# Kernel optimization log

Hardware: AMD Instinct MI355X
Metric: run time of the kernel (lower is better)

## Reference

```python
import jax, jax.numpy as jnp
import numpy as np

B, NN, NC, CARD = 2048, 24, 8, 16
D, H, L, FH, K, DOUT = 512, 8, 3, 1024, 64, 1
S = NN + NC + 1  # M features + CLS token (appended last)
DH = D // H


def _ln(x, w, b):
    m = x.mean(-1, keepdims=True)
    v = ((x - m) ** 2).mean(-1, keepdims=True)
    return (x - m) / jnp.sqrt(v + 1e-5) * w + b


def _build_masks():
    # k random feature-feature interaction pairs per block (seed = attention_seed + block),
    # plus the diagonal and full CLS row/column (CLS is the last token).
    masks = np.zeros((L, S, S), dtype=bool)
    for l in range(L):
        rng = np.random.default_rng(42 + l)
        m = np.zeros((S, S), dtype=bool)
        np.fill_diagonal(m, True)
        m[S - 1, :] = True
        m[:, S - 1] = True
        M = S - 1
        for _ in range(K):
            i, j = rng.integers(0, M, size=2)
            m[i, j] = True
            m[j, i] = True
        masks[l] = m
    return jnp.asarray(masks)


def setup_inputs() -> dict:
    key = jax.random.key(0)
    cnt = [0]

    def nrm(shape, scale=0.02):
        cnt[0] += 1
        return jax.random.normal(jax.random.fold_in(key, cnt[0]), shape, jnp.float32) * scale

    inp = {}
    inp["x_num"] = jax.random.normal(jax.random.fold_in(key, 1000), (B, NN), jnp.float32)
    inp["x_cat"] = jax.random.randint(jax.random.fold_in(key, 1001), (B, NC), 0, CARD)
    # FeatureTokenizer params
    inp["w_num"] = nrm((NN, D), 0.1)
    inp["b_num"] = nrm((NN, D), 0.1)
    inp["emb_cat"] = nrm((NC * CARD, D), 0.1)
    inp["b_cat"] = nrm((NC, D), 0.1)
    inp["cls"] = nrm((D,), 0.1)
    # block params stacked over L blocks
    inp["ln1_w"] = jnp.ones((L, D)); inp["ln1_b"] = jnp.zeros((L, D))
    inp["Wq"] = nrm((L, D, D)); inp["bq"] = jnp.zeros((L, D))
    inp["Wk"] = nrm((L, D, D)); inp["bk"] = jnp.zeros((L, D))
    inp["Wv"] = nrm((L, D, D)); inp["bv"] = jnp.zeros((L, D))
    inp["Wo"] = nrm((L, D, D)); inp["bo"] = jnp.zeros((L, D))
    inp["ln2_w"] = jnp.ones((L, D)); inp["ln2_b"] = jnp.zeros((L, D))
    inp["Wf1"] = nrm((L, D, 2 * FH)); inp["bf1"] = jnp.zeros((L, 2 * FH))
    inp["Wf2"] = nrm((L, FH, D)); inp["bf2"] = jnp.zeros((L, D))
    inp["mask"] = _build_masks()
    inp["cat_offsets"] = jnp.arange(NC) * CARD
    # head params
    inp["hln_w"] = jnp.ones((D,)); inp["hln_b"] = jnp.zeros((D,))
    inp["Wh"] = nrm((D, DOUT)); inp["bh"] = jnp.zeros((DOUT,))
    return inp


def reference(x_num, x_cat, w_num, b_num, emb_cat, b_cat, cls, ln1_w, ln1_b, Wq, bq, Wk, bk, Wv, bv, Wo, bo, ln2_w, ln2_b, Wf1, bf1, Wf2, bf2, mask, cat_offsets, hln_w, hln_b, Wh, bh):
    b = x_num.shape[0]
    tok_num = x_num[:, :, None] * w_num[None] + b_num[None]          # [B, NN, D]
    tok_cat = emb_cat[x_cat + cat_offsets[None]] + b_cat[None]       # [B, NC, D]
    x = jnp.concatenate([tok_num, tok_cat, jnp.broadcast_to(cls, (b, 1, D))], axis=1)  # [B, S, D]
    scale = 1.0 / jnp.sqrt(jnp.asarray(DH, x.dtype))
    for l in range(L):
        # sparse random attention (prenorm)
        h = _ln(x, ln1_w[l], ln1_b[l])
        q = (h @ Wq[l] + bq[l]).reshape(b, S, H, DH)
        k = (h @ Wk[l] + bk[l]).reshape(b, S, H, DH)
        v = (h @ Wv[l] + bv[l]).reshape(b, S, H, DH)
        scores = jnp.einsum('bihd,bjhd->bhij', q, k) * scale
        scores = jnp.where(mask[l][None, None], scores, jnp.asarray(-1e9, scores.dtype))
        attn = jax.nn.softmax(scores, axis=-1)
        o = jnp.einsum('bhij,bjhd->bihd', attn, v).reshape(b, S, D)
        x = x + (o @ Wo[l] + bo[l])
        # ReGLU FFN (prenorm)
        h = _ln(x, ln2_w[l], ln2_b[l])
        f = h @ Wf1[l] + bf1[l]
        a, g = jnp.split(f, 2, axis=-1)
        x = x + ((a * jax.nn.relu(g)) @ Wf2[l] + bf2[l])
    # head on CLS token (last position): LayerNorm -> ReLU -> Linear
    c = _ln(x[:, -1], hln_w, hln_b)
    return jax.nn.relu(c) @ Wh + bh
```

## Files before the change

### kernel.cpp

```cpp
#include <hip/hip_runtime.h>
#include <stdint.h>

#define Bq    2048
#define NNq   24
#define NCq   8
#define CARDq 16
#define Dq    512
#define Hq    8
#define Lq    3
#define FHq   1024
#define Sq    33

typedef unsigned short u16;
typedef unsigned int   u32;
typedef __bf16 bf16x8 __attribute__((ext_vector_type(8)));
typedef float  f32x4  __attribute__((ext_vector_type(4)));

__device__ __forceinline__ u16 f2bf(float f) {
  return __builtin_bit_cast(u16, (__bf16)f);
}
__device__ __forceinline__ float bf2f(u16 h) {
  u32 u = ((u32)h) << 16;
  return __builtin_bit_cast(float, u);
}

__device__ __forceinline__ void glds16(const void* g, void* l) {
  __builtin_amdgcn_global_load_lds((const __attribute__((address_space(1))) void*)g,
                                   (__attribute__((address_space(3))) void*)l, 16, 0, 0);
}

__global__ __launch_bounds__(256) void wconv_all_kernel(const float* __restrict__ Wq,
                                                        const float* __restrict__ Wk,
                                                        const float* __restrict__ Wv,
                                                        const float* __restrict__ Wo,
                                                        const float* __restrict__ Wf1,
                                                        const float* __restrict__ Wf2,
                                                        u16* __restrict__ WqkvT,
                                                        u16* __restrict__ WoT,
                                                        u16* __restrict__ Wf1T,
                                                        u16* __restrict__ Wf2T) {
  __shared__ float tile[32][33];
  const int l = blockIdx.y;
  int id = blockIdx.x;
  const float* src; u16* dst; int K, N;
  if (id < 768) {
    const int m = id >> 8; id &= 255;
    src = ((m == 0) ? Wq : (m == 1) ? Wk : Wv) + (size_t)l * 262144;
    dst = WqkvT + (size_t)l * 786432 + (size_t)m * 262144;
    K = 512; N = 512;
  } else if (id < 1024) {
    id -= 768;
    src = Wo + (size_t)l * 262144;  dst = WoT + (size_t)l * 262144;
    K = 512; N = 512;
  } else if (id < 2048) {
    id -= 1024;
    src = Wf1 + (size_t)l * 1048576; dst = Wf1T + (size_t)l * 1048576;
    K = 512; N = 2048;
  } else {
    id -= 2048;
    src = Wf2 + (size_t)l * 524288;  dst = Wf2T + (size_t)l * 524288;
    K = 1024; N = 512;
  }
  const int ntn = N >> 5;
  const int n0 = (id % ntn) * 32, k0 = (id / ntn) * 32;
  const int tx = threadIdx.x & 31, ty = threadIdx.x >> 5;
#pragma unroll
  for (int r = 0; r < 32; r += 8)
    tile[ty + r][tx] = src[(size_t)(k0 + ty + r) * N + (n0 + tx)];
  __syncthreads();
#pragma unroll
  for (int r = 0; r < 32; r += 8)
    dst[(size_t)(n0 + ty + r) * K + (k0 + tx)] = f2bf(tile[tx][ty + r]);
}

__global__ __launch_bounds__(256) void maskf_kernel(const void* __restrict__ maskp,
                                                    float* __restrict__ maskF) {
  __shared__ int u8flag;
  const int l = blockIdx.x;
  const unsigned char* mu = (const unsigned char*)maskp + (size_t)l * (Sq * Sq);
  const int* mi = (const int*)maskp + (size_t)l * (Sq * Sq);
  if (threadIdx.x == 0) {
    int ok = 1;
    for (int i = 0; i < Sq; i++) ok &= (mu[i * (Sq + 1)] != 0) ? 1 : 0;
    u8flag = ok;
  }
  __syncthreads();
  const int use_u8 = u8flag;
  float* out = maskF + (size_t)l * 2304;
  for (int t = threadIdx.x; t < 2304; t += 256) {
    const int i = t / 48, j = t - i * 48;
    float v = -1e9f;
    if (i < Sq && j < Sq) {
      const int mv = use_u8 ? (int)mu[i * Sq + j] : mi[i * Sq + j];
      v = mv ? 0.f : -1e9f;
    }
    out[t] = v;
  }
}

__global__ __launch_bounds__(256) void tok_ln_kernel(const float* __restrict__ x_num,
                                                     const int* __restrict__ x_cat,
                                                     const float* __restrict__ w_num,
                                                     const float* __restrict__ b_num,
                                                     const float* __restrict__ emb_cat,
                                                     const float* __restrict__ b_cat,
                                                     const float* __restrict__ cls,
                                                     const float* __restrict__ gw,
                                                     const float* __restrict__ gb,
                                                     float* __restrict__ X,
                                                     u16* __restrict__ Hout, int c0) {
  const int wave = threadIdx.x >> 6, lane = threadIdx.x & 63;
  const int tok = blockIdx.x * 4 + wave;
  const int b   = tok / Sq;
  const int s   = tok - b * Sq;
  const int bg  = c0 + b;
  const int col0 = lane * 8;
  float v[8];
  if (s < NNq) {
    const float xv = x_num[bg * NNq + s];
    const float4 w0 = *(const float4*)(w_num + s * Dq + col0);
    const float4 w1 = *(const float4*)(w_num + s * Dq + col0 + 4);
    const float4 b0 = *(const float4*)(b_num + s * Dq + col0);
    const float4 b1 = *(const float4*)(b_num + s * Dq + col0 + 4);
    v[0]=fmaf(xv,w0.x,b0.x); v[1]=fmaf(xv,w0.y,b0.y); v[2]=fmaf(xv,w0.z,b0.z); v[3]=fmaf(xv,w0.w,b0.w);
    v[4]=fmaf(xv,w1.x,b1.x); v[5]=fmaf(xv,w1.y,b1.y); v[6]=fmaf(xv,w1.z,b1.z); v[7]=fmaf(xv,w1.w,b1.w);
  } else if (s < NNq + NCq) {
    const int j = s - NNq;
    const int row = x_cat[bg * NCq + j] + j * CARDq;
    const float4 e0 = *(const float4*)(emb_cat + (size_t)row * Dq + col0);
    const float4 e1 = *(const float4*)(emb_cat + (size_t)row * Dq + col0 + 4);
    const float4 b0 = *(const float4*)(b_cat + j * Dq + col0);
    const float4 b1 = *(const float4*)(b_cat + j * Dq + col0 + 4);
    v[0]=e0.x+b0.x; v[1]=e0.y+b0.y; v[2]=e0.z+b0.z; v[3]=e0.w+b0.w;
    v[4]=e1.x+b1.x; v[5]=e1.y+b1.y; v[6]=e1.z+b1.z; v[7]=e1.w+b1.w;
  } else {
    const float4 c0v = *(const float4*)(cls + col0);
    const float4 c1v = *(const float4*)(cls + col0 + 4);
    v[0]=c0v.x; v[1]=c0v.y; v[2]=c0v.z; v[3]=c0v.w;
    v[4]=c1v.x; v[5]=c1v.y; v[6]=c1v.z; v[7]=c1v.w;
  }
  float s1 = 0.f, s2 = 0.f;
#pragma unroll
  for (int i = 0; i < 8; i++) { s1 += v[i]; s2 += v[i] * v[i]; }
#pragma unroll
  for (int off = 32; off > 0; off >>= 1) { s1 += __shfl_xor(s1, off); s2 += __shfl_xor(s2, off); }
  const float mean = s1 * (1.0f / Dq);
  const float rstd = rsqrtf(s2 * (1.0f / Dq) - mean * mean + 1e-5f);
  float* xp = X + (size_t)tok * Dq + col0;
  *(float4*)xp       = (float4){v[0], v[1], v[2], v[3]};
  *(float4*)(xp + 4) = (float4){v[4], v[5], v[6], v[7]};
  const float* gwp = gw + col0;
  const float* gbp = gb + col0;
  u16 o[8];
#pragma unroll
  for (int i = 0; i < 8; i++) o[i] = f2bf((v[i] - mean) * rstd * gwp[i] + gbp[i]);
  uint4 pk;
  pk.x = (u32)o[0] | ((u32)o[1] << 16); pk.y = (u32)o[2] | ((u32)o[3] << 16);
  pk.z = (u32)o[4] | ((u32)o[5] << 16); pk.w = (u32)o[6] | ((u32)o[7] << 16);
  *(uint4*)(Hout + (size_t)tok * Dq + col0) = pk;
}

__global__ __launch_bounds__(256) void ln_kernel(const float* __restrict__ X,
                                                 const float* __restrict__ gw,
                                                 const float* __restrict__ gb,
                                                 u16* __restrict__ Hout,
                                                 int inmul, int inadd) {
  const int wave = threadIdx.x >> 6, lane = threadIdx.x & 63;
  const int row = blockIdx.x * 4 + wave;
  const size_t srow = (size_t)row * inmul + inadd;
  const float* xr = X + srow * Dq + lane * 8;
  const float4 a = *(const float4*)xr;
  const float4 b = *(const float4*)(xr + 4);
  float s  = a.x + a.y + a.z + a.w + b.x + b.y + b.z + b.w;
  float ss = a.x*a.x + a.y*a.y + a.z*a.z + a.w*a.w + b.x*b.x + b.y*b.y + b.z*b.z + b.w*b.w;
#pragma unroll
  for (int off = 32; off > 0; off >>= 1) { s += __shfl_xor(s, off); ss += __shfl_xor(ss, off); }
  const float mean = s * (1.0f / Dq);
  const float rstd = rsqrtf(ss * (1.0f / Dq) - mean * mean + 1e-5f);
  const float xv[8] = {a.x, a.y, a.z, a.w, b.x, b.y, b.z, b.w};
  const float* gwp = gw + lane * 8;
  const float* gbp = gb + lane * 8;
  u16 o[8];
#pragma unroll
  for (int i = 0; i < 8; i++) o[i] = f2bf((xv[i] - mean) * rstd * gwp[i] + gbp[i]);
  uint4 pk;
  pk.x = (u32)o[0] | ((u32)o[1] << 16); pk.y = (u32)o[2] | ((u32)o[3] << 16);
  pk.z = (u32)o[4] | ((u32)o[5] << 16); pk.w = (u32)o[6] | ((u32)o[7] << 16);
  *(uint4*)(Hout + (size_t)row * Dq + lane * 8) = pk;
}

template <int MODE>
__global__ __launch_bounds__(256) void gemm_kernel(const u16* __restrict__ A,
                                                   const u16* __restrict__ Bt0, const u16* __restrict__ Bt1, const u16* __restrict__ Bt2,
                                                   const float* __restrict__ bi0, const float* __restrict__ bi1, const float* __restrict__ bi2,
                                                   void* __restrict__ out0, void* __restrict__ out1, void* __restrict__ out2,
                                                   size_t ostride, int K, int amul, int aadd, int xmul, int xadd, int nofs) {
  __shared__ uint4 smem4[1024];
  char* smem = (char*)smem4;
  const int tid  = threadIdx.x;
  const int wave = tid >> 6;
  const int lane = tid & 63;
  const int mblk = blockIdx.y;
  const int nblk = blockIdx.x;
  const u16*   Bt;
  const float* bias;
  void*        outp;
  if (MODE == 3) {
    Bt = Bt0; bias = nullptr; outp = out0;
  } else {
    const int z = blockIdx.z;
    Bt   = (z == 0) ? Bt0 : (z == 1) ? Bt1 : Bt2;
    bias = (z == 0) ? bi0 : (z == 1) ? bi1 : bi2;
    outp = (z == 0) ? out0 : (z == 1) ? out1 : out2;
  }

  const int cg   = (lane & 3) ^ ((lane >> 3) & 3);
  const int arow = wave * 32 + (lane >> 2);
  const u16* gA0 = A + ((size_t)(mblk * 128 + arow) * amul + aadd) * K + cg * 8;
  const u16* gA1 = A + ((size_t)(mblk * 128 + arow + 16) * amul + aadd) * K + cg * 8;
  char* lA0 = smem + wave * 2048;
  char* lA1 = lA0 + 1024;

  const u16 *gB0, *gB1;
  char *lB0, *lB1;
  if (MODE == 2) {
    const int brow = wave * 16 + (lane >> 2);
    gB0 = Bt + (size_t)(nblk * 64 + brow) * K + cg * 8;
    gB1 = Bt + (size_t)(FHq + nblk * 64 + brow) * K + cg * 8;
    lB0 = smem + 8192  + wave * 1024;
    lB1 = smem + 12288 + wave * 1024;
  } else {
    const int brow = wave * 32 + (lane >> 2);
    gB0 = Bt + (size_t)((nblk + nofs) * 128 + brow) * K + cg * 8;
    gB1 = gB0 + (size_t)16 * K;
    lB0 = smem + 8192 + wave * 2048;
    lB1 = lB0 + 1024;
  }

  const int slot = (lane >> 4) ^ ((lane >> 1) & 3);
  const int r16  = lane & 15;
  const int wm   = (wave >> 1) * 64;
  int aoff[4], boff[4];
#pragma unroll
  for (int i = 0; i < 4; i++) aoff[i] = (wm + i * 16 + r16) * 64 + slot * 16;
  if (MODE == 2) {
    const int wn = (wave & 1) * 32;
#pragma unroll
    for (int j = 0; j < 2; j++) {
      boff[j]     = 8192  + (wn + j * 16 + r16) * 64 + slot * 16;
      boff[2 + j] = 12288 + (wn + j * 16 + r16) * 64 + slot * 16;
    }
  } else {
    const int wn = (wave & 1) * 64;
#pragma unroll
    for (int j = 0; j < 4; j++) boff[j] = 8192 + (wn + j * 16 + r16) * 64 + slot * 16;
  }

  f32x4 acc[16];
#pragma unroll
  for (int i = 0; i < 16; i++) acc[i] = (f32x4){0.f, 0.f, 0.f, 0.f};

  const int kiter = K >> 5;
  for (int kk = 0; kk < kiter; kk++) {
    __syncthreads();
    glds16(gA0, lA0); glds16(gA1, lA1);
    glds16(gB0, lB0); glds16(gB1, lB1);
    gA0 += 32; gA1 += 32; gB0 += 32; gB1 += 32;
    __syncthreads();

    if (MODE == 2) {
      bf16x8 af[4], ba[2], bg[2];
#pragma unroll
      for (int i = 0; i < 4; i++) af[i] = *(const bf16x8*)(smem + aoff[i]);
#pragma unroll
      for (int j = 0; j < 2; j++) {
        ba[j] = *(const bf16x8*)(smem + boff[j]);
        bg[j] = *(const bf16x8*)(smem + boff[2 + j]);
      }
#pragma unroll
      for (int i = 0; i < 4; i++)
#pragma unroll
        for (int j = 0; j < 2; j++) {
          acc[i * 2 + j]     = __builtin_amdgcn_mfma_f32_16x16x32_bf16(af[i], ba[j], acc[i * 2 + j], 0, 0, 0);
          acc[8 + i * 2 + j] = __builtin_amdgcn_mfma_f32_16x16x32_bf16(af[i], bg[j], acc[8 + i * 2 + j], 0, 0, 0);
        }
    } else {
      bf16x8 af[4], bf[4];
#pragma unroll
      for (int i = 0; i < 4; i++) af[i] = *(const bf16x8*)(smem + aoff[i]);
#pragma unroll
      for (int j = 0; j < 4; j++) bf[j] = *(const bf16x8*)(smem + boff[j]);
#pragma unroll
      for (int i = 0; i < 4; i++)
#pragma unroll
        for (int j = 0; j < 4; j++)
          acc[i * 4 + j] = __builtin_amdgcn_mfma_f32_16x16x32_bf16(af[i], bf[j], acc[i * 4 + j], 0, 0, 0);
    }
  }

  const int quad = lane >> 4;
  if (MODE == 3) {
    const int nb   = nblk + nofs;
    const int buf  = nb >> 2;
    u16* C = (u16*)out0 + (size_t)buf * ostride;
    const float* biasp = (buf == 0) ? bi0 : (buf == 1) ? bi1 : bi2;
    const int colbase = (nb & 3) * 128 + (wave & 1) * 64;
#pragma unroll
    for (int j = 0; j < 4; j++) {
      const int c = colbase + j * 16 + r16;
      const float bv = biasp[c];
#pragma unroll
      for (int i = 0; i < 4; i++) {
        const int r0 = mblk * 128 + wm + i * 16 + quad * 4;
        f32x4 v = acc[i * 4 + j];
#pragma unroll
        for (int r = 0; r < 4; r++)
          C[(size_t)(r0 + r) * Dq + c] = f2bf(v[r] + bv);
      }
    }
  } else if (MODE == 1) {
    float* X = (float*)outp;
    const int wn = (wave & 1) * 64;
#pragma unroll
    for (int j = 0; j < 4; j++) {
      const int c = nblk * 128 + wn + j * 16 + r16;
      const float bv = bias[c];
#pragma unroll
      for (int i = 0; i < 4; i++) {
        const int r0 = mblk * 128 + wm + i * 16 + quad * 4;
        f32x4 v = acc[i * 4 + j];
#pragma unroll
        for (int r = 0; r < 4; r++) {
          const size_t idx = ((size_t)(r0 + r) * xmul + xadd) * Dq + c;
          X[idx] += v[r] + bv;
        }
      }
    }
  } else if (MODE == 2) {
    u16* AG = (u16*)outp;
    const int wn = (wave & 1) * 32;
#pragma unroll
    for (int j = 0; j < 2; j++) {
      const int c = nblk * 64 + wn + j * 16 + r16;
      const float bva = bias[c];
      const float bvg = bias[FHq + c];
#pragma unroll
      for (int i = 0; i < 4; i++) {
        const int r0 = mblk * 128 + wm + i * 16 + quad * 4;
        f32x4 va = acc[i * 2 + j];
        f32x4 vg = acc[8 + i * 2 + j];
#pragma unroll
        for (int r = 0; r < 4; r++) {
          const float av = va[r] + bva;
          const float gv = vg[r] + bvg;
          AG[(size_t)(r0 + r) * FHq + c] = f2bf(av * fmaxf(gv, 0.f));
        }
      }
    }
  }
}

__global__ __launch_bounds__(256) void attn_mfma_kernel(const u16* __restrict__ Q,
                                                        const u16* __restrict__ K,
                                                        const u16* __restrict__ V,
                                                        const float* __restrict__ maskF,
                                                        u16* __restrict__ O) {
  __shared__ u16 lds_all[4][8064];
  const int wave = threadIdx.x >> 6, lane = threadIdx.x & 63;
  const int b = blockIdx.x >> 1;
  const int h = (blockIdx.x & 1) * 4 + wave;
  u16* VT = &lds_all[wave][0];
  u16* P  = &lds_all[wave][64 * 72];
  const size_t hbase = (size_t)b * (Sq * Dq) + (size_t)h * 64;
  const int r16 = lane & 15, quad = lane >> 4;

  const uint4 z4 = {0u, 0u, 0u, 0u};
  for (int t = lane; t < 576; t += 64) ((uint4*)VT)[t] = z4;
  for (int t = lane; t < 432; t += 64) ((uint4*)P)[t]  = z4;
  for (int t = lane; t < 264; t += 64) {
    const int j = t >> 3, ck = t & 7;
    const uint4 src = *(const uint4*)(V + hbase + (size_t)j * Dq + ck * 8);
    const u16* sp = (const u16*)&src;
#pragma unroll
    for (int e = 0; e < 8; e++) VT[(ck * 8 + e) * 72 + j] = sp[e];
  }
  __syncthreads();

  bf16x8 qf[3][2], kf[3][2];
#pragma unroll
  for (int m = 0; m < 3; m++) {
    const int rl = (m * 16 + r16 < Sq) ? (m * 16 + r16) : (Sq - 1);
#pragma unroll
    for (int kk = 0; kk < 2; kk++) {
      qf[m][kk] = *(const bf16x8*)(Q + hbase + (size_t)rl * Dq + kk * 32 + quad * 8);
      kf[m][kk] = *(const bf16x8*)(K + hbase + (size_t)rl * Dq + kk * 32 + quad * 8);
    }
  }
  f32x4 acc[3][3];
#pragma unroll
  for (int m = 0; m < 3; m++)
#pragma unroll
    for (int n = 0; n < 3; n++) acc[m][n] = (f32x4){0.f, 0.f, 0.f, 0.f};
#pragma unroll
  for (int kk = 0; kk < 2; kk++)
#pragma unroll
    for (int m = 0; m < 3; m++)
#pragma unroll
      for (int n = 0; n < 3; n++)
        acc[m][n] = __builtin_amdgcn_mfma_f32_16x16x32_bf16(qf[m][kk], kf[n][kk], acc[m][n], 0, 0, 0);

  float linv[3][4];
#pragma unroll
  for (int m = 0; m < 3; m++) {
    float v[3][4];
#pragma unroll
    for (int n = 0; n < 3; n++) {
      const int c = n * 16 + r16;
#pragma unroll
      for (int r = 0; r < 4; r++) {
        const int R = m * 16 + quad * 4 + r;
        v[n][r] = acc[m][n][r] * 0.125f + maskF[R * 48 + c];
      }
    }
    float mr[4], sum[4];
#pragma unroll
    for (int r = 0; r < 4; r++) {
      mr[r] = fmaxf(fmaxf(v[0][r], v[1][r]), v[2][r]);
#pragma unroll
      for (int off = 8; off > 0; off >>= 1) mr[r] = fmaxf(mr[r], __shfl_xor(mr[r], off));
      sum[r] = 0.f;
    }
#pragma unroll
    for (int n = 0; n < 3; n++)
#pragma unroll
      for (int r = 0; r < 4; r++) { v[n][r] = __expf(v[n][r] - mr[r]); sum[r] += v[n][r]; }
#pragma unroll
    for (int r = 0; r < 4; r++) {
#pragma unroll
      for (int off = 8; off > 0; off >>= 1) sum[r] += __shfl_xor(sum[r], off);
      linv[m][r] = 1.0f / sum[r];
    }
#pragma unroll
    for (int n = 0; n < 3; n++)
#pragma unroll
      for (int r = 0; r < 4; r++)
        P[(m * 16 + quad * 4 + r) * 72 + n * 16 + r16] = f2bf(v[n][r]);
  }
  __syncthreads();

  bf16x8 pa[3][2], vb[4][2];
#pragma unroll
  for (int m = 0; m < 3; m++)
#pragma unroll
    for (int kk = 0; kk < 2; kk++)
      pa[m][kk] = *(const bf16x8*)(P + (m * 16 + r16) * 72 + kk * 32 + quad * 8);
#pragma unroll
  for (int n = 0; n < 4; n++)
#pragma unroll
    for (int kk = 0; kk < 2; kk++)
      vb[n][kk] = *(const bf16x8*)(VT + (n * 16 + r16) * 72 + kk * 32 + quad * 8);
  f32x4 o[3][4];
#pragma unroll
  for (int m = 0; m < 3; m++)
#pragma unroll
    for (int n = 0; n < 4; n++) o[m][n] = (f32x4){0.f, 0.f, 0.f, 0.f};
#pragma unroll
  for (int kk = 0; kk < 2; kk++)
#pragma unroll
    for (int m = 0; m < 3; m++)
#pragma unroll
      for (int n = 0; n < 4; n++)
        o[m][n] = __builtin_amdgcn_mfma_f32_16x16x32_bf16(pa[m][kk], vb[n][kk], o[m][n], 0, 0, 0);

#pragma unroll
  for (int m = 0; m < 3; m++)
#pragma unroll
    for (int r = 0; r < 4; r++) {
      const int i = m * 16 + quad * 4 + r;
      if (i < Sq) {
#pragma unroll
        for (int n = 0; n < 4; n++)
          O[hbase + (size_t)i * Dq + n * 16 + r16] = f2bf(o[m][n][r] * linv[m][r]);
      }
    }
}

__global__ __launch_bounds__(256) void attn_cls_kernel(const u16* __restrict__ Qc,
                                                       const u16* __restrict__ Kf,
                                                       const u16* __restrict__ Vf,
                                                       u16* __restrict__ Oc) {
  __shared__ u16 lds[4][4432];
  __shared__ float psh[4][40];
  const int wave = threadIdx.x >> 6, lane = threadIdx.x & 63;
  const int b = blockIdx.x >> 1;
  const int h = (blockIdx.x & 1) * 4 + wave;
  u16* Kl = &lds[wave][0];
  u16* Vl = &lds[wave][2178];
  u16* ql = &lds[wave][4360];
  const size_t hbase = (size_t)b * (Sq * Dq) + (size_t)h * 64;

  for (int t = lane; t < 528; t += 64) {
    const int mtx = (t >= 264) ? 1 : 0;
    const int e = t - mtx * 264;
    const int j = e >> 3, ck = e & 7;
    const uint4 v = *(const uint4*)((mtx ? Vf : Kf) + hbase + (size_t)j * Dq + ck * 8);
    u16* dst = (mtx ? Vl : Kl) + j * 66 + ck * 8;
    const u16* sp = (const u16*)&v;
#pragma unroll
    for (int e2 = 0; e2 < 8; e2++) dst[e2] = sp[e2];
  }
  if (lane < 8)
    *(uint4*)(ql + lane * 8) = *(const uint4*)(Qc + (size_t)b * Dq + h * 64 + lane * 8);
  __syncthreads();

  float p;
  if (lane < Sq) {
    float s = 0.f;
#pragma unroll 16
    for (int d = 0; d < 64; d++) s += bf2f(ql[d]) * bf2f(Kl[lane * 66 + d]);
    p = s * 0.125f;
  } else p = -3e38f;
  float mx = p;
#pragma unroll
  for (int off = 32; off > 0; off >>= 1) mx = fmaxf(mx, __shfl_xor(mx, off));
  float e = (lane < Sq) ? __expf(p - mx) : 0.f;
  float sum = e;
#pragma unroll
  for (int off = 32; off > 0; off >>= 1) sum += __shfl_xor(sum, off);
  if (lane < Sq) psh[wave][lane] = e / sum;
  __syncthreads();

  float o = 0.f;
#pragma unroll
  for (int j = 0; j < Sq; j++) o += psh[wave][j] * bf2f(Vl[j * 66 + lane]);
  Oc[(size_t)b * Dq + h * 64 + lane] = f2bf(o);
}

__global__ __launch_bounds__(256) void head_kernel(const float* __restrict__ X,
                                                   const float* __restrict__ hw, const float* __restrict__ hb,
                                                   const float* __restrict__ Wh, const float* __restrict__ bh,
                                                   float* __restrict__ out) {
  const int wave = threadIdx.x >> 6, lane = threadIdx.x & 63;
  const int b = blockIdx.x * 4 + wave;
  const float* xr = X + ((size_t)b * Sq + (Sq - 1)) * Dq + lane * 8;
  const float4 a  = *(const float4*)xr;
  const float4 bb = *(const float4*)(xr + 4);
  const float xv[8] = {a.x, a.y, a.z, a.w, bb.x, bb.y, bb.z, bb.w};
  float s = 0.f, ss = 0.f;
#pragma unroll
  for (int i = 0; i < 8; i++) { s += xv[i]; ss += xv[i] * xv[i]; }
#pragma unroll
  for (int off = 32; off > 0; off >>= 1) { s += __shfl_xor(s, off); ss += __shfl_xor(ss, off); }
  const float mean = s * (1.0f / Dq);
  const float rstd = rsqrtf(ss * (1.0f / Dq) - mean * mean + 1e-5f);
  float part = 0.f;
#pragma unroll
  for (int i = 0; i < 8; i++) {
    const float c = (xv[i] - mean) * rstd * hw[lane * 8 + i] + hb[lane * 8 + i];
    part += fmaxf(c, 0.f) * Wh[lane * 8 + i];
  }
#pragma unroll
  for (int off = 32; off > 0; off >>= 1) part += __shfl_xor(part, off);
  if (lane == 0) out[b] = part + bh[0];
}

extern "C" void kernel_launch(void* const* d_in, const int* in_sizes, int n_in,
                              void* d_out, int out_size, void* d_ws, size_t ws_size,
                              hipStream_t stream) {
  (void)in_sizes; (void)n_in; (void)out_size;
  const float* x_num   = (const float*)d_in[0];
  const int*   x_cat   = (const int*)d_in[1];
  const float* w_num   = (const float*)d_in[2];
  const float* b_num   = (const float*)d_in[3];
  const float* emb_cat = (const float*)d_in[4];
  const float* b_cat   = (const float*)d_in[5];
  const float* cls     = (const float*)d_in[6];
  const float* ln1_w   = (const float*)d_in[7];
  const float* ln1_b   = (const float*)d_in[8];
  const float* Wq      = (const float*)d_in[9];
  const float* bq      = (const float*)d_in[10];
  const float* Wk      = (const float*)d_in[11];
  const float* bk      = (const float*)d_in[12];
  const float* Wv      = (const float*)d_in[13];
  const float* bv      = (const float*)d_in[14];
  const float* Wo      = (const float*)d_in[15];
  const float* bo      = (const float*)d_in[16];
  const float* ln2_w   = (const float*)d_in[17];
  const float* ln2_b   = (const float*)d_in[18];
  const float* Wf1     = (const float*)d_in[19];
  const float* bf1     = (const float*)d_in[20];
  const float* Wf2     = (const float*)d_in[21];
  const float* bf2     = (const float*)d_in[22];
  const void*  mask    = d_in[23];
  const float* hln_w   = (const float*)d_in[25];
  const float* hln_b   = (const float*)d_in[26];
  const float* Wh      = (const float*)d_in[27];
  const float* bhp     = (const float*)d_in[28];
  float* out = (float*)d_out;

  const size_t WBYTES = 15728640ULL;
  const size_t MFB    = 27648ULL;
  int Bc = Bq;
  while (Bc > 128) {
    const size_t need = WBYTES + MFB + (size_t)Bc * Sq * 6144ULL;
    if (need <= ws_size) break;
    Bc >>= 1;
  }
  const size_t Mc = (size_t)Bc * Sq;

  char* ws = (char*)d_ws;
  u16* Wbase = (u16*)ws;
  float* maskF = (float*)(ws + WBYTES);
  float* X   = (float*)(ws + WBYTES + MFB);
  u16* Hb    = (u16*)((char*)X + Mc * 2048);
  u16* Qb    = (u16*)((char*)Hb + Mc * 1024);
  u16* Kb    = Qb + Mc * 512;
  u16* Vb    = Kb + Mc * 512;
  u16* AGb   = Qb;

  u16* WqkvT = Wbase;
  u16* WoT   = WqkvT + 2359296;
  u16* Wf1T  = WoT   + 786432;
  u16* Wf2T  = Wf1T  + 3145728;

  wconv_all_kernel<<<dim3(2560, 3), 256, 0, stream>>>(Wq, Wk, Wv, Wo, Wf1, Wf2,
                                                      WqkvT, WoT, Wf1T, Wf2T);
  maskf_kernel<<<Lq, 256, 0, stream>>>(mask, maskF);

  const int mb  = (int)(Mc / 128);
  const int mbC = Bc / 128;

  for (int c0 = 0; c0 < Bq; c0 += Bc) {
    tok_ln_kernel<<<(int)(Mc / 4), 256, 0, stream>>>(x_num, x_cat, w_num, b_num, emb_cat, b_cat, cls,
                                                     ln1_w, ln1_b, X, Hb, c0);

    for (int l = 0; l < Lq; l++) {
      if (l < Lq - 1) {
        gemm_kernel<3><<<dim3(12, mb, 1), 256, 0, stream>>>(Hb,
            WqkvT + l * 786432, nullptr, nullptr,
            bq + l * 512, bk + l * 512, bv + l * 512,
            Qb, nullptr, nullptr, Mc * 512, 512, 1, 0, 1, 0, 0);
        attn_mfma_kernel<<<Bc * 2, 256, 0, stream>>>(Qb, Kb, Vb, maskF + l * 2304, Hb);
        gemm_kernel<1><<<dim3(4, mb, 1), 256, 0, stream>>>(Hb,
            WoT + l * 262144, WoT + l * 262144, WoT + l * 262144,
            bo + l * 512, bo + l * 512, bo + l * 512,
            X, X, X, 0, 512, 1, 0, 1, 0, 0);
        ln_kernel<<<(int)(Mc / 4), 256, 0, stream>>>(X, ln2_w + l * 512, ln2_b + l * 512, Hb, 1, 0);
        gemm_kernel<2><<<dim3(16, mb, 1), 256, 0, stream>>>(Hb,
            Wf1T + l * 1048576, Wf1T + l * 1048576, Wf1T + l * 1048576,
            bf1 + l * 2048, bf1 + l * 2048, bf1 + l * 2048,
            AGb, AGb, AGb, 0, 512, 1, 0, 1, 0, 0);
        gemm_kernel<1><<<dim3(4, mb, 1), 256, 0, stream>>>(AGb,
            Wf2T + l * 524288, Wf2T + l * 524288, Wf2T + l * 524288,
            bf2 + l * 512, bf2 + l * 512, bf2 + l * 512,
            X, X, X, 0, 1024, 1, 0, 1, 0, 0);
        ln_kernel<<<(int)(Mc / 4), 256, 0, stream>>>(X, ln1_w + (l + 1) * 512, ln1_b + (l + 1) * 512, Hb, 1, 0);
      } else {
        gemm_kernel<3><<<dim3(8, mb, 1), 256, 0, stream>>>(Hb,
            WqkvT + l * 786432, nullptr, nullptr,
            bq + l * 512, bk + l * 512, bv + l * 512,
            Qb, nullptr, nullptr, Mc * 512, 512, 1, 0, 1, 0, 4);
        gemm_kernel<3><<<dim3(4, mbC, 1), 256, 0, stream>>>(Hb,
            WqkvT + l * 786432, nullptr, nullptr,
            bq + l * 512, bk + l * 512, bv + l * 512,
            Qb, nullptr, nullptr, Mc * 512, 512, Sq, Sq - 1, 1, 0, 0);
        attn_cls_kernel<<<Bc * 2, 256, 0, stream>>>(Qb, Kb, Vb, Hb);
        gemm_kernel<1><<<dim3(4, mbC, 1), 256, 0, stream>>>(Hb,
            WoT + l * 262144, WoT + l * 262144, WoT + l * 262144,
            bo + l * 512, bo + l * 512, bo + l * 512,
            X, X, X, 0, 512, 1, 0, Sq, Sq - 1, 0);
        ln_kernel<<<Bc / 4, 256, 0, stream>>>(X, ln2_w + l * 512, ln2_b + l * 512, Kb, Sq, Sq - 1);
        gemm_kernel<2><<<dim3(16, mbC, 1), 256, 0, stream>>>(Kb,
            Wf1T + l * 1048576, Wf1T + l * 1048576, Wf1T + l * 1048576,
            bf1 + l * 2048, bf1 + l * 2048, bf1 + l * 2048,
            AGb, AGb, AGb, 0, 512, 1, 0, 1, 0, 0);
        gemm_kernel<1><<<dim3(4, mbC, 1), 256, 0, stream>>>(AGb,
            Wf2T + l * 524288, Wf2T + l * 524288, Wf2T + l * 524288,
            bf2 + l * 512, bf2 + l * 512, bf2 + l * 512,
            X, X, X, 0, 1024, 1, 0, Sq, Sq - 1, 0);
      }
    }
    head_kernel<<<Bc / 4, 256, 0, stream>>>(X, hln_w, hln_b, Wh, bhp, out + c0);
  }
}
```

Baseline: 2.022 ms.

## Restructure attention kernel to one wave per head with coalesced LDS staging

The attention kernel now launches one 64-thread block per (batch, head) instead of four heads per 256-thread block. Q, K and V are loaded with coalesced 16-byte global reads into registers, and Q and K are staged through LDS so the MFMA fragments come from LDS rather than strided global loads. The LDS buffers are then reused for the transposed V and the probability matrix, which cuts LDS per block and should let more blocks stay resident per CU. The trade-offs are more, smaller blocks, extra barriers, a stray no-op LDS read loop, and higher register use to hold V across phases.

```diff
diff --git a/kernel.cpp b/kernel.cpp
--- a/kernel.cpp
+++ b/kernel.cpp
@@ -360,29 +360,40 @@
   }
 }
 
-__global__ __launch_bounds__(256) void attn_mfma_kernel(const u16* __restrict__ Q,
-                                                        const u16* __restrict__ K,
-                                                        const u16* __restrict__ V,
-                                                        const float* __restrict__ maskF,
-                                                        u16* __restrict__ O) {
-  __shared__ u16 lds_all[4][8064];
-  const int wave = threadIdx.x >> 6, lane = threadIdx.x & 63;
-  const int b = blockIdx.x >> 1;
-  const int h = (blockIdx.x & 1) * 4 + wave;
-  u16* VT = &lds_all[wave][0];
-  u16* P  = &lds_all[wave][64 * 72];
+__global__ __launch_bounds__(64) void attn_mfma_kernel(const u16* __restrict__ Q,
+                                                       const u16* __restrict__ K,
+                                                       const u16* __restrict__ V,
+                                                       const float* __restrict__ maskF,
+                                                       u16* __restrict__ O) {
+  __shared__ u16 lds[8064];
+  u16* R1 = lds;
+  u16* R2 = lds + 4608;
+  const int lane = threadIdx.x;
+  const int b = blockIdx.x >> 3;
+  const int h = blockIdx.x & 7;
   const size_t hbase = (size_t)b * (Sq * Dq) + (size_t)h * 64;
   const int r16 = lane & 15, quad = lane >> 4;
 
-  const uint4 z4 = {0u, 0u, 0u, 0u};
-  for (int t = lane; t < 576; t += 64) ((uint4*)VT)[t] = z4;
-  for (int t = lane; t < 432; t += 64) ((uint4*)P)[t]  = z4;
-  for (int t = lane; t < 264; t += 64) {
-    const int j = t >> 3, ck = t & 7;
-    const uint4 src = *(const uint4*)(V + hbase + (size_t)j * Dq + ck * 8);
-    const u16* sp = (const u16*)&src;
-#pragma unroll
-    for (int e = 0; e < 8; e++) VT[(ck * 8 + e) * 72 + j] = sp[e];
+  uint4 qreg[5], kreg[5], vreg[5];
+#pragma unroll
+  for (int it = 0; it < 5; it++) {
+    const int t = lane + it * 64;
+    if (t < 264) {
+      const int j = t >> 3, ck = t & 7;
+      const size_t off = hbase + (size_t)j * Dq + ck * 8;
+      qreg[it] = *(const uint4*)(Q + off);
+      kreg[it] = *(const uint4*)(K + off);
+      vreg[it] = *(const uint4*)(V + off);
+    }
+  }
+#pragma unroll
+  for (int it = 0; it < 5; it++) {
+    const int t = lane + it * 64;
+    if (t < 264) {
+      const int j = t >> 3, ck = t & 7;
+      *(uint4*)(R1 + j * 72 + ck * 8) = kreg[it];
+      *(uint4*)(R2 + j * 72 + ck * 8) = qreg[it];
+    }
   }
   __syncthreads();
 
@@ -392,10 +403,39 @@
     const int rl = (m * 16 + r16 < Sq) ? (m * 16 + r16) : (Sq - 1);
 #pragma unroll
     for (int kk = 0; kk < 2; kk++) {
-      qf[m][kk] = *(const bf16x8*)(Q + hbase + (size_t)rl * Dq + kk * 32 + quad * 8);
-      kf[m][kk] = *(const bf16x8*)(K + hbase + (size_t)rl * Dq + kk * 32 + quad * 8);
-    }
-  }
+      qf[m][kk] = *(const bf16x8*)(R2 + rl * 72 + kk * 32 + quad * 8);
+      kf[m][kk] = *(const bf16x8*)(R1 + rl * 72 + kk * 32 + quad * 8);
+    }
+  }
+  __syncthreads();
+
+  const uint4 z4 = {0u, 0u, 0u, 0u};
+#pragma unroll
+  for (int it = 0; it < 9; it++) ((uint4*)R1)[lane + it * 64];
+#pragma unroll
+  for (int it = 0; it < 9; it++) {
+    const int t = lane + it * 64;
+    if (t < 576) ((uint4*)R1)[t] = z4;
+  }
+#pragma unroll
+  for (int it = 0; it < 5; it++) {
+    const int t = lane + it * 64;
+    if (t < 264) {
+      const int j = t >> 3, ck = t & 7;
+      const u16* sp = (const u16*)&vreg[it];
+#pragma unroll
+      for (int e = 0; e < 8; e++) R1[(ck * 8 + e) * 72 + j] = sp[e];
+    }
+  }
+#pragma unroll
+  for (int it = 0; it < 2; it++) {
+    const int t = lane + it * 64;
+    if (t < 96) {
+      const int row = t >> 1, half = t & 1;
+      *(uint4*)(R2 + row * 72 + 48 + half * 8) = z4;
+    }
+  }
+
   f32x4 acc[3][3];
 #pragma unroll
   for (int m = 0; m < 3; m++)
@@ -444,7 +484,7 @@
     for (int n = 0; n < 3; n++)
 #pragma unroll
       for (int r = 0; r < 4; r++)
-        P[(m * 16 + quad * 4 + r) * 72 + n * 16 + r16] = f2bf(v[n][r]);
+        R2[(m * 16 + quad * 4 + r) * 72 + n * 16 + r16] = f2bf(v[n][r]);
   }
   __syncthreads();
 
@@ -453,12 +493,12 @@
   for (int m = 0; m < 3; m++)
 #pragma unroll
     for (int kk = 0; kk < 2; kk++)
-      pa[m][kk] = *(const bf16x8*)(P + (m * 16 + r16) * 72 + kk * 32 + quad * 8);
+      pa[m][kk] = *(const bf16x8*)(R2 + (m * 16 + r16) * 72 + kk * 32 + quad * 8);
 #pragma unroll
   for (int n = 0; n < 4; n++)
 #pragma unroll
     for (int kk = 0; kk < 2; kk++)
-      vb[n][kk] = *(const bf16x8*)(VT + (n * 16 + r16) * 72 + kk * 32 + quad * 8);
+      vb[n][kk] = *(const bf16x8*)(R1 + (n * 16 + r16) * 72 + kk * 32 + quad * 8);
   f32x4 o[3][4];
 #pragma unroll
   for (int m = 0; m < 3; m++)
@@ -640,7 +680,7 @@
             WqkvT + l * 786432, nullptr, nullptr,
             bq + l * 512, bk + l * 512, bv + l * 512,
             Qb, nullptr, nullptr, Mc * 512, 512, 1, 0, 1, 0, 0);
-        attn_mfma_kernel<<<Bc * 2, 256, 0, stream>>>(Qb, Kb, Vb, maskF + l * 2304, Hb);
+        attn_mfma_kernel<<<Bc * 8, 64, 0, stream>>>(Qb, Kb, Vb, maskF + l * 2304, Hb);
         gemm_kernel<1><<<dim3(4, mb, 1), 256, 0, stream>>>(Hb,
             WoT + l * 262144, WoT + l * 262144, WoT + l * 262144,
             bo + l * 512, bo + l * 512, bo + l * 512,
```

Result: slower. 2.118 ms (+4.7%).
